# Performance work log

Measured on AMD Instinct MI355X. Metric: run time of the kernel, lower is better.

## Reference

```python
import jax, jax.numpy as jnp
import numpy as np

U, I, D = 100000, 200000, 64   # users, items, emb_size
N = U + I                      # total nodes
NNZ = 6400000                  # adjacency non-zeros
B = 4096                       # batch of (user,item) pairs
L = 3                          # n_layers


def setup_inputs() -> dict:
    key = jax.random.key(0)
    ks = jax.random.split(key, 11)
    s = 1.0 / np.sqrt(D)  # xavier-ish scale
    return {
        "user_emb_online": jax.random.normal(ks[0], (U, D), jnp.float32) * s,
        "item_emb_online": jax.random.normal(ks[1], (I, D), jnp.float32) * s,
        "user_emb_target": jax.random.normal(ks[2], (U, D), jnp.float32) * s,
        "item_emb_target": jax.random.normal(ks[3], (I, D), jnp.float32) * s,
        # normalized adjacency values (positive, roughly 1/deg scale)
        "adj_val": jax.random.uniform(ks[4], (NNZ,), jnp.float32) * (1.0 / 16.0),
        "pred_w": jax.random.normal(ks[5], (D, D), jnp.float32) * s,
        "pred_b": jnp.zeros((D,), jnp.float32),
        "adj_row": jax.random.randint(ks[6], (NNZ,), 0, N, dtype=jnp.int32),
        "adj_col": jax.random.randint(ks[7], (NNZ,), 0, N, dtype=jnp.int32),
        "user_idx": jax.random.randint(ks[8], (B,), 0, U, dtype=jnp.int32),
        "item_idx": jax.random.randint(ks[9], (B,), 0, I, dtype=jnp.int32),
    }


def _spmm(row, col, val, x):
    # sparse [N,N] @ dense [N,D] via gather + segment-sum
    return jax.ops.segment_sum(val[:, None] * x[col], row, num_segments=N)


def _lgcn_encode(user_emb, item_emb, row, col, val):
    ego = jnp.concatenate([user_emb, item_emb], axis=0)  # [N, D]
    acc = ego
    x = ego
    for _ in range(L):
        x = _spmm(row, col, val, x)
        acc = acc + x
    all_emb = acc / (L + 1)  # mean over stacked layer outputs
    return all_emb[:U], all_emb[U:]


def reference(user_emb_online, item_emb_online, user_emb_target, item_emb_target,
              adj_val, pred_w, pred_b, adj_row, adj_col, user_idx, item_idx):
    u_on_all, i_on_all = _lgcn_encode(user_emb_online, item_emb_online, adj_row, adj_col, adj_val)
    u_tg_all, i_tg_all = _lgcn_encode(user_emb_target, item_emb_target, adj_row, adj_col, adj_val)
    u_online = u_on_all[user_idx]   # [B, D]
    i_online = i_on_all[item_idx]
    u_target = u_tg_all[user_idx]
    i_target = i_tg_all[item_idx]
    u_pred = u_online @ pred_w.T + pred_b  # nn.Linear
    i_pred = i_online @ pred_w.T + pred_b
    return (u_pred, u_target, i_pred, i_target)
```

## Files before the change

kernel.cpp:

```cpp
#include <hip/hip_runtime.h>
#include <hip/hip_bf16.h>
#include <stdint.h>

#define U_N   100000
#define I_N   200000
#define NN    300000
#define DD    64
#define NNZ_N 6400000
#define BB    4096
#define CHUNK 4096
#define NB    ((NN + CHUNK - 1) / CHUNK)
#define NBK   74
#define EPB   4096
#define NSB   1184
#define SUBCAP 6656
#define BKCAP  94208
#define BKBLK  23
#define LBLK   48000
#define P1B   ((NNZ_N + EPB - 1) / EPB)
#define PACKB ((NN * 16) / 256)
#define ACCB  ((2 * BB * 32) / 256)

typedef unsigned short u16;
typedef unsigned int   u32;
typedef float vf2 __attribute__((ext_vector_type(2)));

__device__ __forceinline__ u16 f2bf(float f) {
    u32 u = __float_as_uint(f);
    u32 r = (u + 0x7FFFu + ((u >> 16) & 1u)) >> 16;
    return (u16)r;
}


#if __has_builtin(__builtin_amdgcn_cvt_pk_f32_fp8) && __has_builtin(__builtin_amdgcn_cvt_pk_fp8_f32)
#define FP8_HW 1
#else
#define FP8_HW 0
#endif

__device__ __forceinline__ u32 enc1_fp8(float f) {
    float af = fabsf(f);
    u32 s = (__float_as_uint(f) >> 31) << 7;
    if (af >= 0.015625f) {
        u32 au = __float_as_uint(af);
        u32 r = au + 0x7FFFFu + ((au >> 20) & 1u);
        u32 e = (r >> 23) - 120u;
        u32 m = (r >> 20) & 7u;
        if (e > 15u) { e = 15u; m = 6u; }
        return s | (e << 3) | m;
    } else {
        u32 q = (u32)__float2int_rn(af * 512.0f);
        return s | q;
    }
}

__device__ __forceinline__ u32 pack4_fp8(float a, float b, float c, float d) {
#if FP8_HW
    u32 w = 0;
    w = (u32)__builtin_amdgcn_cvt_pk_fp8_f32(a, b, (int)w, false);
    w = (u32)__builtin_amdgcn_cvt_pk_fp8_f32(c, d, (int)w, true);
    return w;
#else
    return enc1_fp8(a) | (enc1_fp8(b) << 8) | (enc1_fp8(c) << 16) | (enc1_fp8(d) << 24);
#endif
}

__device__ __forceinline__ float dec1_fp8(u32 b) {
    u32 s = (b & 0x80u) << 24;
    u32 e = (b >> 3) & 15u;
    u32 m = b & 7u;
    float mag = e ? __uint_as_float(((e + 120u) << 23) | (m << 20))
                  : (float)m * 0.001953125f;
    return __uint_as_float(__float_as_uint(mag) | s);
}

__device__ __forceinline__ void dec_fp8x4(u32 w, float* f) {
#if FP8_HW
    vf2 lo = __builtin_amdgcn_cvt_pk_f32_fp8((int)w, false);
    vf2 hi = __builtin_amdgcn_cvt_pk_f32_fp8((int)w, true);
    f[0] = lo[0]; f[1] = lo[1]; f[2] = hi[0]; f[3] = hi[1];
#else
    f[0] = dec1_fp8(w & 255u); f[1] = dec1_fp8((w >> 8) & 255u);
    f[2] = dec1_fp8((w >> 16) & 255u); f[3] = dec1_fp8(w >> 24);
#endif
}


__global__ void setup_k(unsigned char* __restrict__ mark, unsigned char* __restrict__ bmark,
                        int* __restrict__ nlist, int* __restrict__ bkt_cursor) {
    int tid = blockIdx.x * 256 + threadIdx.x;
    if (tid < NN / 4) { ((u32*)mark)[tid] = 0; ((u32*)bmark)[tid] = 0; }
    if (tid < NBK) bkt_cursor[tid] = tid * BKCAP;
    if (tid == NN / 4) nlist[0] = 0;
}


__global__ __launch_bounds__(256) void fused1_k(const int* __restrict__ adj_row,
                                                const int* __restrict__ adj_col,
                                                const float* __restrict__ adj_val,
                                                int* __restrict__ bkt_cursor,
                                                u32* __restrict__ bpk,
                                                float* __restrict__ bval,
                                                const float* __restrict__ ue_on,
                                                const float* __restrict__ ie_on,
                                                const float* __restrict__ ue_tg,
                                                const float* __restrict__ ie_tg,
                                                unsigned char* __restrict__ x0f,
                                                const int* __restrict__ user_idx,
                                                const int* __restrict__ item_idx,
                                                float* __restrict__ out_acc) {
    __shared__ int lcnt[NBK];
    __shared__ int lbase[NBK];
    int bid = blockIdx.x;
    if (bid < P1B) {
        int base = bid * EPB;
        for (int i = threadIdx.x; i < NBK; i += 256) lcnt[i] = 0;
        __syncthreads();
        u32 pk[16]; float vv[16]; int bb[16]; int rk[16];
#pragma unroll
        for (int j = 0; j < 16; j++) {
            int e = base + j * 256 + threadIdx.x;
            bb[j] = -1;
            if (e < NNZ_N) {
                int r = adj_row[e];
                int c = adj_col[e];
                vv[j] = adj_val[e];
                int b = r >> 12;
                pk[j] = ((u32)(r & 4095) << 19) | (u32)c;
                bb[j] = b;
                rk[j] = atomicAdd(&lcnt[b], 1);
            }
        }
        __syncthreads();
        for (int i = threadIdx.x; i < NBK; i += 256)
            lbase[i] = atomicAdd(&bkt_cursor[i], lcnt[i]);
        __syncthreads();
#pragma unroll
        for (int j = 0; j < 16; j++) {
            if (bb[j] >= 0) {
                int p = lbase[bb[j]] + rk[j];
                bpk[p]  = pk[j];
                bval[p] = vv[j];
            }
        }
        return;
    }
    bid -= P1B;
    if (bid < PACKB) {
        int tid = bid * 256 + threadIdx.x;
        int n = tid >> 4;
        int t = tid & 15;
        if (n >= NN) return;
        const float* src;
        int soff;
        if (t < 8) {
            soff = t * 8;
            src = (n < U_N) ? ue_on + (size_t)n * 64 : ie_on + (size_t)(n - U_N) * 64;
        } else {
            soff = (t - 8) * 8;
            src = (n < U_N) ? ue_tg + (size_t)n * 64 : ie_tg + (size_t)(n - U_N) * 64;
        }
        float4 f0 = *(const float4*)(src + soff);
        float4 f1 = *(const float4*)(src + soff + 4);
        uint2 o;
        o.x = pack4_fp8(f0.x, f0.y, f0.z, f0.w);
        o.y = pack4_fp8(f1.x, f1.y, f1.z, f1.w);
        *(uint2*)(x0f + (size_t)n * 128 + t * 8) = o;
        return;
    }
    bid -= PACKB;
    {
        int t = bid * 256 + threadIdx.x;
        int slot = t >> 5;
        int j = t & 31;
        if (slot >= 2 * BB) return;
        int node = (slot < BB) ? user_idx[slot] : U_N + item_idx[slot - BB];
        const float* src;
        int soff, doff;
        if (j < 16) {
            soff = j * 4; doff = j * 4;
            src = (node < U_N) ? ue_on + (size_t)node * 64 : ie_on + (size_t)(node - U_N) * 64;
        } else {
            soff = (j - 16) * 4; doff = 64 + (j - 16) * 4;
            src = (node < U_N) ? ue_tg + (size_t)node * 64 : ie_tg + (size_t)(node - U_N) * 64;
        }
        float4 f = *(const float4*)(src + soff);
        *(float4*)(out_acc + (size_t)slot * 128 + doff) = f;
    }
}


__global__ __launch_bounds__(1024) void fused2_k(const int* __restrict__ bkt_cursor,
                                                 const u32* __restrict__ bpk,
                                                 int* __restrict__ cnt,
                                                 int* __restrict__ bsums,
                                                 int* __restrict__ row_ptr) {
    if (blockIdx.x < NBK) {
        __shared__ int h[4096];
        int b = blockIdx.x;
        int base = b * BKCAP;
        int e1 = bkt_cursor[b];
        for (int j = threadIdx.x; j < 4096; j += 1024) h[j] = 0;
        __syncthreads();
        for (int i = base + threadIdx.x; i < e1; i += 1024)
            atomicAdd(&h[bpk[i] >> 19], 1);
        __syncthreads();
        int rb = b << 12;
        for (int j = threadIdx.x; j < 4096; j += 1024) {
            int idx = rb + j;
            if (idx < NN) cnt[idx] = h[j];
        }
    } else {
        __shared__ int sh[128];
        int t = threadIdx.x;
        int v = 0;
        if (t < 128) {
            v = (t < NB) ? bkt_cursor[t] - t * BKCAP : 0;
            sh[t] = v;
        }
        __syncthreads();
        for (int o = 1; o < 128; o <<= 1) {
            int tmp = 0;
            if (t < 128 && t >= o) tmp = sh[t - o];
            __syncthreads();
            if (t < 128) sh[t] += tmp;
            __syncthreads();
        }
        if (t < NB) bsums[t] = sh[t] - v;
        if (t == 127) row_ptr[NN] = sh[127];
    }
}

__global__ void scan3_k(const int* __restrict__ cnt, const int* __restrict__ bsums,
                        int* __restrict__ row_ptr, int* __restrict__ sub_cursor) {
    __shared__ int tsum[256];
    int base = blockIdx.x * CHUNK;
    int loc[16];
    int s = 0;
#pragma unroll
    for (int j = 0; j < 16; j++) {
        int idx = base + threadIdx.x * 16 + j;
        int c = (idx < NN) ? cnt[idx] : 0;
        loc[j] = s;
        s += c;
    }
    tsum[threadIdx.x] = s;
    __syncthreads();
    int v = s;
    for (int o = 1; o < 256; o <<= 1) {
        int t = (threadIdx.x >= o) ? tsum[threadIdx.x - o] : 0;
        __syncthreads();
        tsum[threadIdx.x] += t;
        __syncthreads();
    }
    int texcl = tsum[threadIdx.x] - v;
    int boff = bsums[blockIdx.x];
#pragma unroll
    for (int j = 0; j < 16; j++) {
        int idx = base + threadIdx.x * 16 + j;
        if (idx < NN) {
            int val = boff + texcl + loc[j];
            row_ptr[idx] = val;
            if ((idx & 255) == 0) sub_cursor[idx >> 8] = val;
        }
    }
}


__global__ __launch_bounds__(256) void p2r_k(const int* __restrict__ bkt_cursor,
                                             const u32* __restrict__ bpk,
                                             const float* __restrict__ bval,
                                             int* __restrict__ sub_cursor,
                                             int2* __restrict__ mid) {
    __shared__ int lcnt[16], lbase[16], sbase[16];
    __shared__ int2 stage[4096];
    int b = blockIdx.y;
    int e1 = bkt_cursor[b];
    int base = b * BKCAP + blockIdx.x * 4096;
    if (base >= e1) return;
    if (threadIdx.x < 16) lcnt[threadIdx.x] = 0;
    __syncthreads();
    u32 pk[16]; float vv[16]; int sb[16], rk[16];
#pragma unroll
    for (int j = 0; j < 16; j++) {
        int e = base + j * 256 + threadIdx.x;
        sb[j] = -1;
        if (e < e1) {
            pk[j] = bpk[e];
            vv[j] = bval[e];
            int s = (int)((pk[j] >> 27) & 15u);
            sb[j] = s;
            rk[j] = atomicAdd(&lcnt[s], 1);
        }
    }
    __syncthreads();
    if (threadIdx.x == 0) {
        int acc = 0;
#pragma unroll
        for (int s = 0; s < 16; s++) { sbase[s] = acc; acc += lcnt[s]; }
    }
    if (threadIdx.x < 16)
        lbase[threadIdx.x] = atomicAdd(&sub_cursor[b * 16 + threadIdx.x], lcnt[threadIdx.x]);
    __syncthreads();
#pragma unroll
    for (int j = 0; j < 16; j++)
        if (sb[j] >= 0)
            stage[sbase[sb[j]] + rk[j]] = make_int2((int)pk[j], __float_as_int(vv[j]));
    __syncthreads();
    for (int s = 0; s < 16; s++) {
        int c = lcnt[s], gb = lbase[s], lb = sbase[s];
        for (int i = threadIdx.x; i < c; i += 256)
            mid[gb + i] = stage[lb + i];
    }
}


__global__ __launch_bounds__(256) void p3_k(const int* __restrict__ row_ptr,
                                            const int2* __restrict__ mid,
                                            int2* __restrict__ edge_s) {
    __shared__ int rbase[256], rcur[256];
    __shared__ int2 stage[SUBCAP];
    int s = blockIdx.x;
    int r0 = s << 8;
    if (r0 >= NN) return;
    int r1 = min(r0 + 256, NN);
    int nr = r1 - r0;
    int ebase = row_ptr[r0];
    int eend  = row_ptr[r1];
    int cnt = eend - ebase;
    if (threadIdx.x < nr) {
        rbase[threadIdx.x] = row_ptr[r0 + threadIdx.x] - ebase;
        rcur[threadIdx.x] = 0;
    }
    __syncthreads();
    for (int i = threadIdx.x; i < cnt; i += 256) {
        int2 d = mid[ebase + i];
        u32 pk = (u32)d.x;
        int l = (int)((pk >> 19) & 255u);
        int pos = rbase[l] + atomicAdd(&rcur[l], 1);
        if (pos < SUBCAP) stage[pos] = make_int2((int)(pk & 0x7FFFFu), d.y);
    }
    __syncthreads();
    for (int i = threadIdx.x; i < cnt; i += 256) edge_s[ebase + i] = stage[i];
}


__global__ void mark_k(const int* __restrict__ row_ptr, const int2* __restrict__ edge_s,
                       const int* __restrict__ user_idx, const int* __restrict__ item_idx,
                       unsigned char* __restrict__ mark, unsigned char* __restrict__ bmark) {
    int wave = threadIdx.x >> 6;
    int lane = threadIdx.x & 63;
    int slot = blockIdx.x * 4 + wave;
    if (slot >= 2 * BB) return;
    int r = (slot < BB) ? user_idx[slot] : U_N + item_idx[slot - BB];
    if (lane == 0) { mark[r] = 1; bmark[r] = 1; }
    int e0 = row_ptr[r], e1 = row_ptr[r + 1];
    for (int e = e0 + lane; e < e1; e += 64) mark[edge_s[e].x] = 1;
}

__global__ void compact_k(const unsigned char* __restrict__ mark,
                          int* __restrict__ list2, int* __restrict__ nlist) {
    int i = blockIdx.x * 256 + threadIdx.x;
    int lane = threadIdx.x & 63;
    int m = (i < NN) ? (int)mark[i] : 0;
    unsigned long long b = __ballot(m != 0);
    int pre = __popcll(b & ((1ull << lane) - 1ull));
    int tot = __popcll(b);
    int base = 0;
    if (lane == 0 && tot) base = atomicAdd(nlist, tot);
    base = __shfl(base, 0);
    if (m) list2[base + pre] = i;
}


struct acc8 { float a[8]; };

__device__ __forceinline__ void red8(acc8& A) {
#pragma unroll
    for (int k = 0; k < 8; k++) {
        A.a[k] += __shfl_xor(A.a[k], 16);
        A.a[k] += __shfl_xor(A.a[k], 32);
    }
}

__device__ __forceinline__ void rg8_core(const int2* __restrict__ edge_s,
                                         const unsigned char* __restrict__ xf,
                                         int t, int g, int e0, int e1, acc8& A) {
#pragma unroll
    for (int k = 0; k < 8; k++) A.a[k] = 0.f;
    const unsigned char* xt = xf + t * 8;
    int d = e1 - e0;

    int2 ed[8];
    uint2 pv[8];
#pragma unroll
    for (int q = 0; q < 8; q++) { ed[q] = make_int2(0, 0); pv[q] = make_uint2(0u, 0u); }
#pragma unroll
    for (int q = 0; q < 8; q++) {
        int j = g + 4 * q;
        if (j < d) ed[q] = edge_s[e0 + j];
    }
#pragma unroll
    for (int q = 0; q < 8; q++) {
        int j = g + 4 * q;
        if (j < d) pv[q] = *(const uint2*)(xt + (size_t)((u32)ed[q].x * 128u));
    }
#pragma unroll
    for (int q = 0; q < 8; q++) {
        float v = __int_as_float(ed[q].y);
        float f[8];
        dec_fp8x4(pv[q].x, f);
        dec_fp8x4(pv[q].y, f + 4);
#pragma unroll
        for (int k = 0; k < 8; k++) A.a[k] += v * f[k];
    }
    for (int e = e0 + 32 + g * 4; e < e1; e += 16) {
        int m = e1 - e;
#pragma unroll
        for (int k = 0; k < 4; k++) {
            if (k < m) {
                int2 dd = edge_s[e + k];
                float v = __int_as_float(dd.y);
                uint2 p = *(const uint2*)(xt + (size_t)((u32)dd.x * 128u));
                float f[8];
                dec_fp8x4(p.x, f);
                dec_fp8x4(p.y, f + 4);
#pragma unroll
                for (int q = 0; q < 8; q++) A.a[q] += v * f[q];
            }
        }
    }
    red8(A);
}

__global__ __launch_bounds__(256) void spmm1_k(const int* __restrict__ row_ptr,
                                               const int2* __restrict__ edge_s,
                                               const unsigned char* __restrict__ x0f,
                                               const unsigned char* __restrict__ bmark,
                                               u16* __restrict__ y,
                                               unsigned char* __restrict__ yf) {
    int lane = threadIdx.x & 63;
    int t = lane & 15, g = lane >> 4;
    int r = blockIdx.x * 4 + (threadIdx.x >> 6);
    if (r >= NN) return;
    acc8 A;
    rg8_core(edge_s, x0f, t, g, row_ptr[r], row_ptr[r + 1], A);
    if (g == 0) {
        uint2 of;
        of.x = pack4_fp8(A.a[0], A.a[1], A.a[2], A.a[3]);
        of.y = pack4_fp8(A.a[4], A.a[5], A.a[6], A.a[7]);
        *(uint2*)(yf + (size_t)r * 128 + t * 8) = of;
        if (bmark[r]) {
            uint4 o;
            o.x = ((u32)f2bf(A.a[1]) << 16) | (u32)f2bf(A.a[0]);
            o.y = ((u32)f2bf(A.a[3]) << 16) | (u32)f2bf(A.a[2]);
            o.z = ((u32)f2bf(A.a[5]) << 16) | (u32)f2bf(A.a[4]);
            o.w = ((u32)f2bf(A.a[7]) << 16) | (u32)f2bf(A.a[6]);
            *(uint4*)(y + (size_t)r * 128 + t * 8) = o;
        }
    }
}

__device__ __forceinline__ void rg16_core(const int2* __restrict__ edge_s,
                                          const u16* __restrict__ x,
                                          int t, int g, int e0, int e1, acc8& A) {
#pragma unroll
    for (int k = 0; k < 8; k++) A.a[k] = 0.f;
    const u16* xt = x + t * 8;
    int d = e1 - e0;

    int2 ed[8];
    uint4 pv[8];
#pragma unroll
    for (int q = 0; q < 8; q++) { ed[q] = make_int2(0, 0); pv[q] = make_uint4(0u, 0u, 0u, 0u); }
#pragma unroll
    for (int q = 0; q < 8; q++) {
        int j = g + 4 * q;
        if (j < d) ed[q] = edge_s[e0 + j];
    }
#pragma unroll
    for (int q = 0; q < 8; q++) {
        int j = g + 4 * q;
        if (j < d) pv[q] = *(const uint4*)(xt + (size_t)(u32)ed[q].x * 128);
    }
#pragma unroll
    for (int q = 0; q < 8; q++) {
        float v = __int_as_float(ed[q].y);
        A.a[0] += v * __uint_as_float(pv[q].x << 16);
        A.a[1] += v * __uint_as_float(pv[q].x & 0xFFFF0000u);
        A.a[2] += v * __uint_as_float(pv[q].y << 16);
        A.a[3] += v * __uint_as_float(pv[q].y & 0xFFFF0000u);
        A.a[4] += v * __uint_as_float(pv[q].z << 16);
        A.a[5] += v * __uint_as_float(pv[q].z & 0xFFFF0000u);
        A.a[6] += v * __uint_as_float(pv[q].w << 16);
        A.a[7] += v * __uint_as_float(pv[q].w & 0xFFFF0000u);
    }
    for (int e = e0 + 32 + g * 4; e < e1; e += 16) {
        int m = e1 - e;
#pragma unroll
        for (int k = 0; k < 4; k++) {
            if (k < m) {
                int2 dd = edge_s[e + k];
                float v = __int_as_float(dd.y);
                uint4 p = *(const uint4*)(xt + (size_t)(u32)dd.x * 128);
                A.a[0] += v * __uint_as_float(p.x << 16);
                A.a[1] += v * __uint_as_float(p.x & 0xFFFF0000u);
                A.a[2] += v * __uint_as_float(p.y << 16);
                A.a[3] += v * __uint_as_float(p.y & 0xFFFF0000u);
                A.a[4] += v * __uint_as_float(p.z << 16);
                A.a[5] += v * __uint_as_float(p.z & 0xFFFF0000u);
                A.a[6] += v * __uint_as_float(p.w << 16);
                A.a[7] += v * __uint_as_float(p.w & 0xFFFF0000u);
            }
        }
    }
    red8(A);
}

__global__ __launch_bounds__(256) void spmm_list_k(const int* __restrict__ row_ptr,
                                                   const int2* __restrict__ edge_s,
                                                   const unsigned char* __restrict__ x1f,
                                                   u16* __restrict__ y,
                                                   const int* __restrict__ list2,
                                                   const int* __restrict__ nlist) {
    int lane = threadIdx.x & 63;
    int t = lane & 15, g = lane >> 4;
    int slot = blockIdx.x * 4 + (threadIdx.x >> 6);
    if (slot >= *nlist) return;
    int r = list2[slot];
    acc8 A;
    rg8_core(edge_s, x1f, t, g, row_ptr[r], row_ptr[r + 1], A);
    if (g == 0) {
        uint4 o;
        o.x = ((u32)f2bf(A.a[1]) << 16) | (u32)f2bf(A.a[0]);
        o.y = ((u32)f2bf(A.a[3]) << 16) | (u32)f2bf(A.a[2]);
        o.z = ((u32)f2bf(A.a[5]) << 16) | (u32)f2bf(A.a[4]);
        o.w = ((u32)f2bf(A.a[7]) << 16) | (u32)f2bf(A.a[6]);
        *(uint4*)(y + (size_t)r * 128 + t * 8) = o;
    }
}

__global__ __launch_bounds__(256) void spmm_last_k(const int* __restrict__ row_ptr,
                                                   const int2* __restrict__ edge_s,
                                                   const u16* __restrict__ x,
                                                   const int* __restrict__ user_idx,
                                                   const int* __restrict__ item_idx,
                                                   float* __restrict__ out_acc) {
    int lane = threadIdx.x & 63;
    int t = lane & 15, g = lane >> 4;
    int slot = blockIdx.x * 4 + (threadIdx.x >> 6);
    if (slot >= 2 * BB) return;
    int r = (slot < BB) ? user_idx[slot] : U_N + item_idx[slot - BB];
    acc8 A;
    rg16_core(edge_s, x, t, g, row_ptr[r], row_ptr[r + 1], A);
    if (g == 0) {
        uint4 p = *(const uint4*)(x + (size_t)r * 128 + t * 8);
        A.a[0] += __uint_as_float(p.x << 16);
        A.a[1] += __uint_as_float(p.x & 0xFFFF0000u);
        A.a[2] += __uint_as_float(p.y << 16);
        A.a[3] += __uint_as_float(p.y & 0xFFFF0000u);
        A.a[4] += __uint_as_float(p.z << 16);
        A.a[5] += __uint_as_float(p.z & 0xFFFF0000u);
        A.a[6] += __uint_as_float(p.w << 16);
        A.a[7] += __uint_as_float(p.w & 0xFFFF0000u);
        float4* p0 = (float4*)(out_acc + (size_t)slot * 128 + t * 8);
        float4 c0 = p0[0], c1 = p0[1];
        c0.x += A.a[0]; c0.y += A.a[1]; c0.z += A.a[2]; c0.w += A.a[3];
        c1.x += A.a[4]; c1.y += A.a[5]; c1.z += A.a[6]; c1.w += A.a[7];
        p0[0] = c0; p0[1] = c1;
    }
}


__global__ void gadd_k(const int* __restrict__ user_idx, const int* __restrict__ item_idx,
                       const u16* __restrict__ x, float* __restrict__ out_acc) {
    int t = blockIdx.x * blockDim.x + threadIdx.x;
    int slot = t >> 6;
    int l = t & 63;
    if (slot >= 2 * BB) return;
    int node = (slot < BB) ? user_idx[slot] : U_N + item_idx[slot - BB];
    u32 p = *(const u32*)(x + (size_t)node * 128 + (l << 1));
    float fx = __uint_as_float(p << 16);
    float fy = __uint_as_float(p & 0xFFFF0000u);
    float2* q = (float2*)(out_acc + (size_t)slot * 128) + l;
    float2 cur = *q;
    cur.x += fx; cur.y += fy;
    *q = cur;
}


__global__ __launch_bounds__(256) void pred_k(const float* __restrict__ out_acc,
                                              const float* __restrict__ W,
                                              const float* __restrict__ bias,
                                              float* __restrict__ out) {
    __shared__ float wld[64 * 65];
    __shared__ float uld[4 * 64];
    int j = threadIdx.x & 63;
    int rl = threadIdx.x >> 6;
    for (int i = threadIdx.x; i < 4096; i += 256) {
        int jj = i >> 6, kk = i & 63;
        wld[kk * 65 + jj] = W[i];
    }
    int slot = blockIdx.x * 4 + rl;
    uld[rl * 64 + j] = out_acc[(size_t)slot * 128 + j] * 0.25f;
    float tv = out_acc[(size_t)slot * 128 + 64 + j] * 0.25f;
    size_t tdst = (slot < BB) ? (size_t)BB * 64 + (size_t)slot * 64 + j
                              : (size_t)3 * BB * 64 + (size_t)(slot - BB) * 64 + j;
    out[tdst] = tv;
    __syncthreads();
    float acc = bias[j];
#pragma unroll
    for (int k = 0; k < 64; k++) acc += uld[rl * 64 + k] * wld[k * 65 + j];
    size_t dst = (slot < BB) ? (size_t)slot * 64 + j
                             : (size_t)2 * BB * 64 + (size_t)(slot - BB) * 64 + j;
    out[dst] = acc;
}


extern "C" void kernel_launch(void* const* d_in, const int* in_sizes, int n_in,
                              void* d_out, int out_size, void* d_ws, size_t ws_size,
                              hipStream_t stream) {
    const float* ue_on = (const float*)d_in[0];
    const float* ie_on = (const float*)d_in[1];
    const float* ue_tg = (const float*)d_in[2];
    const float* ie_tg = (const float*)d_in[3];
    const float* adj_val = (const float*)d_in[4];
    const float* pred_w = (const float*)d_in[5];
    const float* pred_b = (const float*)d_in[6];
    const int* adj_row = (const int*)d_in[7];
    const int* adj_col = (const int*)d_in[8];
    const int* user_idx = (const int*)d_in[9];
    const int* item_idx = (const int*)d_in[10];
    float* out = (float*)d_out;

    char* ws = (char*)d_ws;
    size_t off = 0;
    auto alloc = [&](size_t bytes) -> char* {
        char* p = ws + off;
        off = (off + bytes + 255) & ~(size_t)255;
        return p;
    };
    int*   cnt        = (int*)alloc((size_t)NN * 4);
    int*   row_ptr    = (int*)alloc((size_t)(NN + 1) * 4);
    int*   bsums      = (int*)alloc(256 * 4);
    int*   bkt_cursor = (int*)alloc(256 * 4);
    int*   sub_cursor = (int*)alloc((size_t)NSB * 4);
    unsigned char* mark = (unsigned char*)alloc((size_t)NN);
    unsigned char* bmark = (unsigned char*)alloc((size_t)NN);
    int*   list2      = (int*)alloc((size_t)NN * 4);
    int*   nlist      = (int*)alloc(256 * 4);
    int2*  edge_s     = (int2*)alloc((size_t)NNZ_N * 8);
    u16*   x_a        = (u16*)alloc((size_t)NN * 128 * 2);
    u16*   x_b        = (u16*)alloc((size_t)NN * 128 * 2);
    float* out_acc    = (float*)alloc((size_t)2 * BB * 128 * 4);

    unsigned char* x0f = (unsigned char*)x_a;
    unsigned char* x1f = (unsigned char*)x_a + (size_t)NN * 128;
    float* bval = (float*)x_b;
    u32*   bpk  = (u32*)((char*)x_b + (size_t)NN * 128);
    int2*  mid  = edge_s;

    (void)n_in; (void)in_sizes; (void)out_size; (void)ws_size;

    setup_k<<<294, 256, 0, stream>>>(mark, bmark, nlist, bkt_cursor);
    fused1_k<<<P1B + PACKB + ACCB, 256, 0, stream>>>(adj_row, adj_col, adj_val,
                                                     bkt_cursor, bpk, bval,
                                                     ue_on, ie_on, ue_tg, ie_tg, x0f,
                                                     user_idx, item_idx, out_acc);
    fused2_k<<<NBK + 1, 1024, 0, stream>>>(bkt_cursor, bpk, cnt, bsums, row_ptr);
    scan3_k<<<NB, 256, 0, stream>>>(cnt, bsums, row_ptr, sub_cursor);
    p2r_k<<<dim3(BKBLK, NBK), 256, 0, stream>>>(bkt_cursor, bpk, bval, sub_cursor, mid);
    p3_k<<<NSB, 256, 0, stream>>>(row_ptr, mid, edge_s);

    mark_k<<<(2 * BB) / 4, 256, 0, stream>>>(row_ptr, edge_s, user_idx, item_idx, mark, bmark);
    compact_k<<<(NN + 255) / 256, 256, 0, stream>>>(mark, list2, nlist);

    spmm1_k<<<NN / 4, 256, 0, stream>>>(row_ptr, edge_s, x0f, bmark, x_b, x1f);
    gadd_k<<<(2 * BB * 64) / 256, 256, 0, stream>>>(user_idx, item_idx, x_b, out_acc);
    spmm_list_k<<<LBLK, 256, 0, stream>>>(row_ptr, edge_s, x1f, x_b, list2, nlist);
    spmm_last_k<<<(2 * BB) / 4, 256, 0, stream>>>(row_ptr, edge_s, x_b, user_idx, item_idx, out_acc);

    pred_k<<<(2 * BB) / 4, 256, 0, stream>>>(out_acc, pred_w, pred_b, out);
}
```

Measured before the change: 738.4 us.

## Fuse CSR construction into a single per-bucket histogram, scan and scatter kernel

Rows are now bucketed by 1024 instead of 4096, with 293 buckets. A single bsort_k kernel replaces the four-kernel chain fused2/scan3/p2r/p3. Each 1024-thread block redundantly scans all bucket counts to find its global base, builds a row histogram in shared memory, scans it to write row_ptr, and scatters edges straight into edge_s using shared-memory atomic cursors. This removes three launches, the intermediate mid array pass and the cnt/bsums buffers, in exchange for uncoalesced scatter writes within each bucket's range and a bucket capacity limit of 25088 edges per 1024 rows.

```diff
diff --git a/kernel.cpp b/kernel.cpp
--- a/kernel.cpp
+++ b/kernel.cpp
@@ -8,15 +8,11 @@
 #define DD    64
 #define NNZ_N 6400000
 #define BB    4096
-#define CHUNK 4096
-#define NB    ((NN + CHUNK - 1) / CHUNK)
-#define NBK   74
+#define RPB   1024
+#define NBK   293
 #define EPB   4096
-#define NSB   1184
-#define SUBCAP 6656
-#define BKCAP  94208
-#define BKBLK  23
-#define LBLK   48000
+#define BKCAP 25088
+#define LBLK  48000
 #define P1B   ((NNZ_N + EPB - 1) / EPB)
 #define PACKB ((NN * 16) / 256)
 #define ACCB  ((2 * BB * 32) / 256)
@@ -125,8 +121,8 @@
                 int r = adj_row[e];
                 int c = adj_col[e];
                 vv[j] = adj_val[e];
-                int b = r >> 12;
-                pk[j] = ((u32)(r & 4095) << 19) | (u32)c;
+                int b = r >> 10;
+                pk[j] = ((u32)(r & 1023) << 19) | (u32)c;
                 bb[j] = b;
                 rk[j] = atomicAdd(&lcnt[b], 1);
             }
@@ -190,158 +186,56 @@
 }
 
 
-__global__ __launch_bounds__(1024) void fused2_k(const int* __restrict__ bkt_cursor,
-                                                 const u32* __restrict__ bpk,
-                                                 int* __restrict__ cnt,
-                                                 int* __restrict__ bsums,
-                                                 int* __restrict__ row_ptr) {
-    if (blockIdx.x < NBK) {
-        __shared__ int h[4096];
-        int b = blockIdx.x;
-        int base = b * BKCAP;
-        int e1 = bkt_cursor[b];
-        for (int j = threadIdx.x; j < 4096; j += 1024) h[j] = 0;
-        __syncthreads();
-        for (int i = base + threadIdx.x; i < e1; i += 1024)
-            atomicAdd(&h[bpk[i] >> 19], 1);
-        __syncthreads();
-        int rb = b << 12;
-        for (int j = threadIdx.x; j < 4096; j += 1024) {
-            int idx = rb + j;
-            if (idx < NN) cnt[idx] = h[j];
-        }
-    } else {
-        __shared__ int sh[128];
-        int t = threadIdx.x;
-        int v = 0;
-        if (t < 128) {
-            v = (t < NB) ? bkt_cursor[t] - t * BKCAP : 0;
-            sh[t] = v;
-        }
-        __syncthreads();
-        for (int o = 1; o < 128; o <<= 1) {
-            int tmp = 0;
-            if (t < 128 && t >= o) tmp = sh[t - o];
-            __syncthreads();
-            if (t < 128) sh[t] += tmp;
-            __syncthreads();
-        }
-        if (t < NB) bsums[t] = sh[t] - v;
-        if (t == 127) row_ptr[NN] = sh[127];
-    }
-}
-
-__global__ void scan3_k(const int* __restrict__ cnt, const int* __restrict__ bsums,
-                        int* __restrict__ row_ptr, int* __restrict__ sub_cursor) {
-    __shared__ int tsum[256];
-    int base = blockIdx.x * CHUNK;
-    int loc[16];
-    int s = 0;
-#pragma unroll
-    for (int j = 0; j < 16; j++) {
-        int idx = base + threadIdx.x * 16 + j;
-        int c = (idx < NN) ? cnt[idx] : 0;
-        loc[j] = s;
-        s += c;
-    }
-    tsum[threadIdx.x] = s;
+__global__ __launch_bounds__(1024) void bsort_k(const int* __restrict__ bkt_cursor,
+                                                const u32* __restrict__ bpk,
+                                                const float* __restrict__ bval,
+                                                int2* __restrict__ edge_s,
+                                                int* __restrict__ row_ptr) {
+    __shared__ int h[RPB];
+    __shared__ int bs[512];
+    int b = blockIdx.x;
+    int t = threadIdx.x;
+    int base = b * BKCAP;
+    int e1 = bkt_cursor[b];
+    int v = 0;
+    if (t < 512) {
+        v = (t < NBK) ? bkt_cursor[t] - t * BKCAP : 0;
+        bs[t] = v;
+    }
+    h[t] = 0;
     __syncthreads();
-    int v = s;
-    for (int o = 1; o < 256; o <<= 1) {
-        int t = (threadIdx.x >= o) ? tsum[threadIdx.x - o] : 0;
-        __syncthreads();
-        tsum[threadIdx.x] += t;
-        __syncthreads();
-    }
-    int texcl = tsum[threadIdx.x] - v;
-    int boff = bsums[blockIdx.x];
-#pragma unroll
-    for (int j = 0; j < 16; j++) {
-        int idx = base + threadIdx.x * 16 + j;
-        if (idx < NN) {
-            int val = boff + texcl + loc[j];
-            row_ptr[idx] = val;
-            if ((idx & 255) == 0) sub_cursor[idx >> 8] = val;
-        }
-    }
-}
-
-
-__global__ __launch_bounds__(256) void p2r_k(const int* __restrict__ bkt_cursor,
-                                             const u32* __restrict__ bpk,
-                                             const float* __restrict__ bval,
-                                             int* __restrict__ sub_cursor,
-                                             int2* __restrict__ mid) {
-    __shared__ int lcnt[16], lbase[16], sbase[16];
-    __shared__ int2 stage[4096];
-    int b = blockIdx.y;
-    int e1 = bkt_cursor[b];
-    int base = b * BKCAP + blockIdx.x * 4096;
-    if (base >= e1) return;
-    if (threadIdx.x < 16) lcnt[threadIdx.x] = 0;
+    for (int o = 1; o < 512; o <<= 1) {
+        int tmp = 0;
+        if (t < 512 && t >= o) tmp = bs[t - o];
+        __syncthreads();
+        if (t < 512) bs[t] += tmp;
+        __syncthreads();
+    }
+    int bucket_base = (b == 0) ? 0 : bs[b - 1];
+    if (b == NBK - 1 && t == 0) row_ptr[NN] = bs[NBK - 1];
+    for (int i = base + t; i < e1; i += 1024)
+        atomicAdd(&h[bpk[i] >> 19], 1);
     __syncthreads();
-    u32 pk[16]; float vv[16]; int sb[16], rk[16];
-#pragma unroll
-    for (int j = 0; j < 16; j++) {
-        int e = base + j * 256 + threadIdx.x;
-        sb[j] = -1;
-        if (e < e1) {
-            pk[j] = bpk[e];
-            vv[j] = bval[e];
-            int s = (int)((pk[j] >> 27) & 15u);
-            sb[j] = s;
-            rk[j] = atomicAdd(&lcnt[s], 1);
-        }
-    }
+    int hv = h[t];
+    for (int o = 1; o < 1024; o <<= 1) {
+        int tmp = (t >= o) ? h[t - o] : 0;
+        __syncthreads();
+        h[t] += tmp;
+        __syncthreads();
+    }
+    int excl = h[t] - hv;
+    int r = b * RPB + t;
+    if (r < NN) row_ptr[r] = bucket_base + excl;
     __syncthreads();
-    if (threadIdx.x == 0) {
-        int acc = 0;
-#pragma unroll
-        for (int s = 0; s < 16; s++) { sbase[s] = acc; acc += lcnt[s]; }
-    }
-    if (threadIdx.x < 16)
-        lbase[threadIdx.x] = atomicAdd(&sub_cursor[b * 16 + threadIdx.x], lcnt[threadIdx.x]);
+    h[t] = bucket_base + excl;
     __syncthreads();
-#pragma unroll
-    for (int j = 0; j < 16; j++)
-        if (sb[j] >= 0)
-            stage[sbase[sb[j]] + rk[j]] = make_int2((int)pk[j], __float_as_int(vv[j]));
-    __syncthreads();
-    for (int s = 0; s < 16; s++) {
-        int c = lcnt[s], gb = lbase[s], lb = sbase[s];
-        for (int i = threadIdx.x; i < c; i += 256)
-            mid[gb + i] = stage[lb + i];
-    }
-}
-
-
-__global__ __launch_bounds__(256) void p3_k(const int* __restrict__ row_ptr,
-                                            const int2* __restrict__ mid,
-                                            int2* __restrict__ edge_s) {
-    __shared__ int rbase[256], rcur[256];
-    __shared__ int2 stage[SUBCAP];
-    int s = blockIdx.x;
-    int r0 = s << 8;
-    if (r0 >= NN) return;
-    int r1 = min(r0 + 256, NN);
-    int nr = r1 - r0;
-    int ebase = row_ptr[r0];
-    int eend  = row_ptr[r1];
-    int cnt = eend - ebase;
-    if (threadIdx.x < nr) {
-        rbase[threadIdx.x] = row_ptr[r0 + threadIdx.x] - ebase;
-        rcur[threadIdx.x] = 0;
-    }
-    __syncthreads();
-    for (int i = threadIdx.x; i < cnt; i += 256) {
-        int2 d = mid[ebase + i];
-        u32 pk = (u32)d.x;
-        int l = (int)((pk >> 19) & 255u);
-        int pos = rbase[l] + atomicAdd(&rcur[l], 1);
-        if (pos < SUBCAP) stage[pos] = make_int2((int)(pk & 0x7FFFFu), d.y);
-    }
-    __syncthreads();
-    for (int i = threadIdx.x; i < cnt; i += 256) edge_s[ebase + i] = stage[i];
+    for (int i = base + t; i < e1; i += 1024) {
+        u32 pk = bpk[i];
+        float vv = bval[i];
+        int l = (int)(pk >> 19);
+        int pos = atomicAdd(&h[l], 1);
+        edge_s[pos] = make_int2((int)(pk & 0x7FFFFu), __float_as_int(vv));
+    }
 }
 
 
@@ -640,11 +534,8 @@
         off = (off + bytes + 255) & ~(size_t)255;
         return p;
     };
-    int*   cnt        = (int*)alloc((size_t)NN * 4);
     int*   row_ptr    = (int*)alloc((size_t)(NN + 1) * 4);
-    int*   bsums      = (int*)alloc(256 * 4);
-    int*   bkt_cursor = (int*)alloc(256 * 4);
-    int*   sub_cursor = (int*)alloc((size_t)NSB * 4);
+    int*   bkt_cursor = (int*)alloc(512 * 4);
     unsigned char* mark = (unsigned char*)alloc((size_t)NN);
     unsigned char* bmark = (unsigned char*)alloc((size_t)NN);
     int*   list2      = (int*)alloc((size_t)NN * 4);
@@ -658,7 +549,6 @@
     unsigned char* x1f = (unsigned char*)x_a + (size_t)NN * 128;
     float* bval = (float*)x_b;
     u32*   bpk  = (u32*)((char*)x_b + (size_t)NN * 128);
-    int2*  mid  = edge_s;
 
     (void)n_in; (void)in_sizes; (void)out_size; (void)ws_size;
 
@@ -667,10 +557,7 @@
                                                      bkt_cursor, bpk, bval,
                                                      ue_on, ie_on, ue_tg, ie_tg, x0f,
                                                      user_idx, item_idx, out_acc);
-    fused2_k<<<NBK + 1, 1024, 0, stream>>>(bkt_cursor, bpk, cnt, bsums, row_ptr);
-    scan3_k<<<NB, 256, 0, stream>>>(cnt, bsums, row_ptr, sub_cursor);
-    p2r_k<<<dim3(BKBLK, NBK), 256, 0, stream>>>(bkt_cursor, bpk, bval, sub_cursor, mid);
-    p3_k<<<NSB, 256, 0, stream>>>(row_ptr, mid, edge_s);
+    bsort_k<<<NBK, 1024, 0, stream>>>(bkt_cursor, bpk, bval, edge_s, row_ptr);
 
     mark_k<<<(2 * BB) / 4, 256, 0, stream>>>(row_ptr, edge_s, user_idx, item_idx, mark, bmark);
     compact_k<<<(NN + 255) / 256, 256, 0, stream>>>(mark, list2, nlist);
```

Result: slower. 814.7 us (+10.3%).
